# Performance work log

Measured on AMD Instinct MI355X. Metric: run time of the kernel, lower is better.

The kernel has to match this reference:

```python
import jax, jax.numpy as jnp
import numpy as np

MINVAL = 0.0
MAXVAL = 1.0
G = 4096   # grid_dim
C = 8      # channels
N = 4      # batch


def setup_inputs() -> dict:
    key = jax.random.key(0)
    k1, k2 = jax.random.split(key)
    # uniform 1-D grid on [0, 1) -> dx = 1/G (get_dx(grid))
    grid = jnp.arange(G, dtype=jnp.float32) / G
    density = jax.random.normal(k1, (N, 1, G), dtype=jnp.float32)
    # nn.Parameter xi initialized with nn.init.uniform_ -> U[0, 1)
    xi = jax.random.uniform(k2, (C,), dtype=jnp.float32)
    return {"density": density, "xi": xi, "grid": grid}


def reference(density, xi, grid):
    # density: (N, 1, G); xi: (C,); grid: (G,)
    dx = grid[1] - grid[0]                                   # uniform spacing
    g = jnp.abs(grid[:, None] - grid[None, :])               # (G, G) pairwise |x_i - x_j|
    xi_eff = 1.0 / (MINVAL + (MAXVAL - MINVAL) * jax.nn.sigmoid(xi))  # (C,)
    expo = jnp.exp(-g[None, :, :] * xi_eff[:, None, None])   # (C, G, G) dense kernel
    # 'i, jkl, ilm -> jim': sum over singleton channel k of density and grid dim l
    integral = jnp.einsum('i,jkl,ilm->jim', 0.5 * xi_eff, density, expo)  # (N, C, G)
    return integral * dx
```

## Files before the change

### kernel.cpp

```cpp
#include <hip/hip_runtime.h>


#define GG 4096
#define CC 8
#define NN 4
#define BLOCK 256
#define CHUNK (GG / BLOCK)

__global__ __launch_bounds__(BLOCK) void gconv_scan(const float* __restrict__ density,
                                                    const float* __restrict__ xi,
                                                    const float* __restrict__ grid,
                                                    float* __restrict__ out) {
    const int bid  = blockIdx.x;
    const int c    = bid & (CC - 1);
    const int n    = bid >> 3;
    const int tid  = threadIdx.x;
    const int base = tid * CHUNK;

    const float k  = 1.0f + expf(-xi[c]);
    const float dx = grid[1] - grid[0];

    const float4* dv4 = reinterpret_cast<const float4*>(density + n * GG + base);
    const float4* gv4 = reinterpret_cast<const float4*>(grid + base);

    float ea[CHUNK];
    float eb[CHUNK];
    float pa[CHUNK];
    float sb[CHUNK];

    float runA = 0.0f;
#pragma unroll
    for (int q = 0; q < CHUNK / 4; ++q) {
        float4 d4 = dv4[q];
        float4 g4 = gv4[q];
        float xs[4] = {g4.x, g4.y, g4.z, g4.w};
        float ds[4] = {d4.x, d4.y, d4.z, d4.w};
#pragma unroll
        for (int j = 0; j < 4; ++j) {
            const int i = q * 4 + j;
            const float e  = expf(xs[j] * k);
            const float ei = expf(-xs[j] * k);
            ea[i] = e;
            eb[i] = ei;
            runA += ds[j] * e;
            pa[i] = runA;
            sb[i] = ds[j] * ei;
        }
    }
    float runB = 0.0f;
#pragma unroll
    for (int i = CHUNK - 1; i >= 0; --i) {
        const float bv = sb[i];
        sb[i] = runB;
        runB += bv;
    }

    float sA = runA, sB = runB;
#pragma unroll
    for (int off = 1; off < 64; off <<= 1) {
        const float tA = __shfl_up(sA, off, 64);
        const float tB = __shfl_up(sB, off, 64);
        if ((tid & 63) >= off) { sA += tA; sB += tB; }
    }

    __shared__ float wA[BLOCK / 64];
    __shared__ float wB[BLOCK / 64];
    const int wave = tid >> 6;
    if ((tid & 63) == 63) { wA[wave] = sA; wB[wave] = sB; }
    __syncthreads();

    float preA = 0.0f, preB = 0.0f, totB = 0.0f;
#pragma unroll
    for (int w = 0; w < BLOCK / 64; ++w) {
        const float ta = wA[w];
        const float tb = wB[w];
        if (w < wave) { preA += ta; preB += tb; }
        totB += tb;
    }
    const float offA = preA + (sA - runA);
    const float offB = totB - (preB + sB);

    const float scale = 0.5f * k * dx;
    float4* o4 = reinterpret_cast<float4*>(out + bid * GG + base);
#pragma unroll
    for (int q = 0; q < CHUNK / 4; ++q) {
        float4 r;
        float* rp = &r.x;
#pragma unroll
        for (int j = 0; j < 4; ++j) {
            const int i = q * 4 + j;
            const float A = offA + pa[i];
            const float B = offB + sb[i];
            rp[j] = scale * (eb[i] * A + ea[i] * B);
        }
        o4[q] = r;
    }
}

extern "C" void kernel_launch(void* const* d_in, const int* in_sizes, int n_in,
                              void* d_out, int out_size, void* d_ws, size_t ws_size,
                              hipStream_t stream) {
    const float* density = (const float*)d_in[0];
    const float* xi      = (const float*)d_in[1];
    const float* grid    = (const float*)d_in[2];
    float* out           = (float*)d_out;

    gconv_scan<<<NN * CC, BLOCK, 0, stream>>>(density, xi, grid, out);
}
```

Measured before the change: 59.03 us.

## Split scan into two-pass segmented reduce-then-scan across many blocks

Replaces the single-block-per-(n,c) scan, where each thread serially handles 16 elements, with a two-kernel scheme over 16 segments per combo. The first kernel reduces per-segment sums of d·e^{xk} and d·e^{-xk} into the workspace. The second recomputes the exponentials, adds the preceding and following segment totals, and does an in-block prefix and suffix scan to produce outputs. This raises the block count from 32 to 512 to fill more compute units. The cost is a second launch, recomputed exponentials, and a workspace round trip.

```diff
diff --git a/kernel.cpp b/kernel.cpp
--- a/kernel.cpp
+++ b/kernel.cpp
@@ -4,97 +4,106 @@
 #define GG 4096
 #define CC 8
 #define NN 4
+#define SS 16
+#define SEG (GG / SS)
 #define BLOCK 256
-#define CHUNK (GG / BLOCK)
+#define NCOMBO (NN * CC)
+#define NBLK (NCOMBO * SS)
 
-__global__ __launch_bounds__(BLOCK) void gconv_scan(const float* __restrict__ density,
+__global__ __launch_bounds__(BLOCK) void gconv_part(const float* __restrict__ density,
                                                     const float* __restrict__ xi,
                                                     const float* __restrict__ grid,
-                                                    float* __restrict__ out) {
-    const int bid  = blockIdx.x;
-    const int c    = bid & (CC - 1);
-    const int n    = bid >> 3;
-    const int tid  = threadIdx.x;
-    const int base = tid * CHUNK;
+                                                    float* __restrict__ ws) {
+    const int bid   = blockIdx.x;
+    const int seg   = bid & (SS - 1);
+    const int combo = bid >> 4;
+    const int c     = combo & (CC - 1);
+    const int n     = combo >> 3;
+    const int tid   = threadIdx.x;
+    const int g     = seg * SEG + tid;
+
+    const float k  = 1.0f + expf(-xi[c]);
+    const float x  = grid[g];
+    const float d  = density[n * GG + g];
+    const float xk = x * k;
+    float sA = d * expf(xk);
+    float sB = d * expf(-xk);
+
+#pragma unroll
+    for (int off = 32; off > 0; off >>= 1) {
+        sA += __shfl_xor(sA, off, 64);
+        sB += __shfl_xor(sB, off, 64);
+    }
+    __shared__ float wA[BLOCK / 64], wB[BLOCK / 64];
+    const int wave = tid >> 6;
+    if ((tid & 63) == 0) { wA[wave] = sA; wB[wave] = sB; }
+    __syncthreads();
+    if (tid == 0) {
+        ws[bid]        = wA[0] + wA[1] + wA[2] + wA[3];
+        ws[NBLK + bid] = wB[0] + wB[1] + wB[2] + wB[3];
+    }
+}
+
+__global__ __launch_bounds__(BLOCK) void gconv_out(const float* __restrict__ density,
+                                                   const float* __restrict__ xi,
+                                                   const float* __restrict__ grid,
+                                                   const float* __restrict__ ws,
+                                                   float* __restrict__ out) {
+    const int bid   = blockIdx.x;
+    const int seg   = bid & (SS - 1);
+    const int combo = bid >> 4;
+    const int c     = combo & (CC - 1);
+    const int n     = combo >> 3;
+    const int tid   = threadIdx.x;
+    const int lane  = tid & 63;
+    const int wave  = tid >> 6;
+    const int g     = seg * SEG + tid;
 
     const float k  = 1.0f + expf(-xi[c]);
     const float dx = grid[1] - grid[0];
+    const float x  = grid[g];
+    const float d  = density[n * GG + g];
+    const float xk = x * k;
+    const float ea = expf(xk);
+    const float eb = expf(-xk);
+    const float a  = d * ea;
+    const float b  = d * eb;
 
-    const float4* dv4 = reinterpret_cast<const float4*>(density + n * GG + base);
-    const float4* gv4 = reinterpret_cast<const float4*>(grid + base);
-
-    float ea[CHUNK];
-    float eb[CHUNK];
-    float pa[CHUNK];
-    float sb[CHUNK];
-
-    float runA = 0.0f;
+    const float* TA = ws + combo * SS;
+    const float* TB = ws + NBLK + combo * SS;
+    float offA = 0.0f, offB = 0.0f;
 #pragma unroll
-    for (int q = 0; q < CHUNK / 4; ++q) {
-        float4 d4 = dv4[q];
-        float4 g4 = gv4[q];
-        float xs[4] = {g4.x, g4.y, g4.z, g4.w};
-        float ds[4] = {d4.x, d4.y, d4.z, d4.w};
-#pragma unroll
-        for (int j = 0; j < 4; ++j) {
-            const int i = q * 4 + j;
-            const float e  = expf(xs[j] * k);
-            const float ei = expf(-xs[j] * k);
-            ea[i] = e;
-            eb[i] = ei;
-            runA += ds[j] * e;
-            pa[i] = runA;
-            sb[i] = ds[j] * ei;
-        }
-    }
-    float runB = 0.0f;
-#pragma unroll
-    for (int i = CHUNK - 1; i >= 0; --i) {
-        const float bv = sb[i];
-        sb[i] = runB;
-        runB += bv;
+    for (int s = 0; s < SS; ++s) {
+        const float ta = TA[s];
+        const float tb = TB[s];
+        if (s < seg) offA += ta;
+        if (s > seg) offB += tb;
     }
 
-    float sA = runA, sB = runB;
+    float pa = a, sb = b;
 #pragma unroll
     for (int off = 1; off < 64; off <<= 1) {
-        const float tA = __shfl_up(sA, off, 64);
-        const float tB = __shfl_up(sB, off, 64);
-        if ((tid & 63) >= off) { sA += tA; sB += tB; }
+        const float tA = __shfl_up(pa, off, 64);
+        if (lane >= off) pa += tA;
+        const float tB = __shfl_down(sb, off, 64);
+        if (lane + off < 64) sb += tB;
     }
 
-    __shared__ float wA[BLOCK / 64];
-    __shared__ float wB[BLOCK / 64];
-    const int wave = tid >> 6;
-    if ((tid & 63) == 63) { wA[wave] = sA; wB[wave] = sB; }
+    __shared__ float wTA[BLOCK / 64], wTB[BLOCK / 64];
+    if (lane == 63) wTA[wave] = pa;
+    if (lane == 0)  wTB[wave] = sb;
     __syncthreads();
-
-    float preA = 0.0f, preB = 0.0f, totB = 0.0f;
+    float wOffA = 0.0f, wOffB = 0.0f;
 #pragma unroll
     for (int w = 0; w < BLOCK / 64; ++w) {
-        const float ta = wA[w];
-        const float tb = wB[w];
-        if (w < wave) { preA += ta; preB += tb; }
-        totB += tb;
+        if (w < wave) wOffA += wTA[w];
+        if (w > wave) wOffB += wTB[w];
     }
-    const float offA = preA + (sA - runA);
-    const float offB = totB - (preB + sB);
 
+    const float A = offA + wOffA + pa;
+    const float B = offB + wOffB + (sb - b);
     const float scale = 0.5f * k * dx;
-    float4* o4 = reinterpret_cast<float4*>(out + bid * GG + base);
-#pragma unroll
-    for (int q = 0; q < CHUNK / 4; ++q) {
-        float4 r;
-        float* rp = &r.x;
-#pragma unroll
-        for (int j = 0; j < 4; ++j) {
-            const int i = q * 4 + j;
-            const float A = offA + pa[i];
-            const float B = offB + sb[i];
-            rp[j] = scale * (eb[i] * A + ea[i] * B);
-        }
-        o4[q] = r;
-    }
+    out[(n * CC + c) * GG + g] = scale * (eb * A + ea * B);
 }
 
 extern "C" void kernel_launch(void* const* d_in, const int* in_sizes, int n_in,
@@ -104,6 +113,8 @@
     const float* xi      = (const float*)d_in[1];
     const float* grid    = (const float*)d_in[2];
     float* out           = (float*)d_out;
+    float* ws            = (float*)d_ws;
 
-    gconv_scan<<<NN * CC, BLOCK, 0, stream>>>(density, xi, grid, out);
+    gconv_part<<<NBLK, BLOCK, 0, stream>>>(density, xi, grid, ws);
+    gconv_out<<<NBLK, BLOCK, 0, stream>>>(density, xi, grid, ws, out);
 }
```

Measured after the change: 60.68 us. +2.8%, slower.
